# Performance work log

Measured on AMD Instinct MI355X. Metric: run time of the kernel, lower is better.

Reference implementation:

```python
import jax, jax.numpy as jnp
import numpy as np

NEG_INF = 1e9  # matches module's -1000000000.0 masking constant


def setup_inputs() -> dict:
    key = jax.random.key(0)
    kq, kv = jax.random.split(key)
    B, T, D = 4, 2048, 1024
    query = jax.random.normal(kq, (B, T, D), dtype=jnp.float32)
    value = jax.random.normal(kv, (B, T, D), dtype=jnp.float32)
    return {"query": query, "value": value}


def reference(query, value):
    # key defaults to value (len(inputs) == 2 path)
    k = value
    # dot-product scores (canonical Keras Attention _calculate_scores)
    scores = jnp.einsum("bqd,bkd->bqk", query, k)  # [B, Tq, Tv]
    Tq, Tv = scores.shape[-2], scores.shape[-1]
    # causal lower-triangular mask over last two dims (row >= col)
    causal_mask = jnp.tril(jnp.ones((Tq, Tv), dtype=bool))  # [Tq, Tv]
    # scores -= 1e9 * (~mask), then softmax (eval mode: no dropout)
    scores = scores - NEG_INF * (~causal_mask).astype(scores.dtype)
    weights = jax.nn.softmax(scores, axis=-1)
    result = jnp.einsum("bqv,bvd->bqd", weights, value)
    return result
```

## Files before the change

### kernel.cpp

```cpp
#include <hip/hip_runtime.h>
#include <hip/hip_fp16.h>

typedef _Float16 half8 __attribute__((ext_vector_type(8)));
typedef _Float16 half2v __attribute__((ext_vector_type(2)));
typedef float    floatx4 __attribute__((ext_vector_type(4)));

#define MFMA16(a, b, c) __builtin_amdgcn_mfma_f32_16x16x32_f16((a), (b), (c), 0, 0, 0)

constexpr int T_ = 2048;
constexpr int D_ = 1024;
constexpr int NB = 4;
constexpr int NTILE = 136;
constexpr size_t TILE_ELEMS = 16384;

__device__ __forceinline__ half8 cvt8(floatx4 a, floatx4 b) {
  half8 h;
  h[0] = (_Float16)a[0]; h[1] = (_Float16)a[1]; h[2] = (_Float16)a[2]; h[3] = (_Float16)a[3];
  h[4] = (_Float16)b[0]; h[5] = (_Float16)b[1]; h[6] = (_Float16)b[2]; h[7] = (_Float16)b[3];
  return h;
}

__device__ __forceinline__ void gl16(const void* g, void* l) {
  __builtin_amdgcn_global_load_lds(
      (const __attribute__((address_space(1))) void*)g,
      (__attribute__((address_space(3))) void*)l, 16, 0, 0);
}

__global__ __launch_bounds__(256) void cast_q(const float* __restrict__ Q,
                                              _Float16* __restrict__ Qh) {
  const size_t e = ((size_t)blockIdx.x * 256 + threadIdx.x) * 8;
  const int t = (int)(e >> 10);
  const int c = (int)((e >> 3) & 127);
  const int cd = (c & ~7) | ((c ^ t) & 7);
  half8 h = cvt8(*(const floatx4*)(Q + e), *(const floatx4*)(Q + e + 4));
  *(half8*)(Qh + ((size_t)t << 10) + (cd << 3)) = h;
}

__global__ __launch_bounds__(256) void build_vt(const float* __restrict__ V,
                                                _Float16* __restrict__ VhT) {
  __shared__ _Float16 tile[64][65];
  const int bid = blockIdx.x;
  const int b = bid & 3, tt = (bid >> 2) & 31, dd = bid >> 7;
  const float* Vb = V + ((size_t)b * T_ + tt * 64) * D_ + dd * 64;
#pragma unroll
  for (int k = 0; k < 16; ++k) {
    const int e = k * 256 + threadIdx.x, r = e >> 6, c = e & 63;
    tile[r][c] = (_Float16)Vb[(size_t)r * D_ + c];
  }
  __syncthreads();
#pragma unroll
  for (int k = 0; k < 16; ++k) {
    const int e = k * 256 + threadIdx.x, dr = e >> 6, tc = e & 63;
    const int tcd = ((((tc >> 3) ^ dr) & 7) << 3) | (tc & 7);
    VhT[((size_t)b * D_ + dd * 64 + dr) * T_ + tt * 64 + tcd] = tile[tc][dr];
  }
}

__global__ __launch_bounds__(256, 3) void sgemm(const _Float16* __restrict__ Qh,
                                                const float* __restrict__ V,
                                                float* __restrict__ Sp) {
  __shared__ __align__(16) char As[16384];
  __shared__ __align__(16) char Bs[32768];
  const int tid = threadIdx.x;
  const int w = tid >> 6, l = tid & 63, l15 = l & 15, hi = l >> 4;
  const int wr = (w >> 1) * 64, wc = (w & 1) * 64;

  const int b = (int)(blockIdx.x & 3);
  int rem = (int)(blockIdx.x >> 2), j = 0;
  while (rem >= 16 - j) { rem -= 16 - j; ++j; }
  const int i = j + rem;

  const int arow = w * 32 + (l >> 3);
  const int brow = w * 32 + (l >> 4);
  const _Float16* Asrc = Qh + ((size_t)(b * T_ + i * 128 + arow)) * D_ + (l & 7) * 8;
  const float* Bb = V + ((size_t)(b * T_ + j * 128 + brow)) * D_;
  const int lc0 = (l & 8) | ((l & 7) ^ (l >> 4));
  char* Adst = As + w * 4096;
  char* Bdst = Bs + w * 8192;

  floatx4 acc[4][4];
#pragma unroll
  for (int mi = 0; mi < 4; ++mi)
#pragma unroll
    for (int ni = 0; ni < 4; ++ni) acc[mi][ni] = (floatx4){0.f, 0.f, 0.f, 0.f};

  for (int s = 0; s < 16; ++s) {
#pragma unroll
    for (int q = 0; q < 4; ++q)
      gl16(Asrc + (size_t)q * 8 * D_ + s * 64, Adst + q * 1024);
#pragma unroll
    for (int q = 0; q < 8; ++q)
      gl16(Bb + (size_t)q * 4 * D_ + s * 64 + (lc0 ^ ((q & 1) << 2)) * 4,
           Bdst + q * 1024);
    __syncthreads();
#pragma unroll
    for (int s32 = 0; s32 < 2; ++s32) {
      half8 af[4], bb[4];
#pragma unroll
      for (int mi = 0; mi < 4; ++mi) {
        const int row = wr + mi * 16 + l15;
        af[mi] = *(const half8*)(As + row * 128 + ((((s32 << 2) | hi) ^ (row & 7)) << 4));
      }
#pragma unroll
      for (int ni = 0; ni < 4; ++ni) {
        const int row = wc + ni * 16 + l15;
        const int p0 = (s32 << 3) | (((hi << 1) ^ row) & 7);
        const floatx4 f0 = *(const floatx4*)(Bs + row * 256 + (p0 << 4));
        const floatx4 f1 = *(const floatx4*)(Bs + row * 256 + ((p0 ^ 1) << 4));
        bb[ni] = cvt8(f0, f1);
      }
#pragma unroll
      for (int mi = 0; mi < 4; ++mi)
#pragma unroll
        for (int ni = 0; ni < 4; ++ni)
          acc[mi][ni] = MFMA16(af[mi], bb[ni], acc[mi][ni]);
    }
    __syncthreads();
  }

  float* tp = Sp + (size_t)(b * NTILE + ((i * (i + 1)) >> 1) + j) * TILE_ELEMS;
#pragma unroll
  for (int mi = 0; mi < 4; ++mi)
#pragma unroll
    for (int r = 0; r < 4; ++r) {
      const int row = wr + mi * 16 + 4 * hi + r;
#pragma unroll
      for (int ni = 0; ni < 4; ++ni)
        tp[row * 128 + wc + ni * 16 + l15] = acc[mi][ni][r];
    }
}

__global__ __launch_bounds__(256) void smax(float* __restrict__ Sp,
                                            float* __restrict__ lrow) {
  const int b = (int)(blockIdx.x & 3), t = (int)(blockIdx.x >> 2);
  const int i = 15 - (t >> 5), rg = t & 31;
  const int w = threadIdx.x >> 6, l = threadIdx.x & 63;
  const int r = rg * 4 + w, m = i * 128 + r, len = m + 1;
  char* tb0 = (char*)(Sp + (size_t)(b * NTILE + ((i * (i + 1)) >> 1)) * TILE_ELEMS);

  float mx = -1e30f;
  for (int j = 0; j <= i; ++j) {
    const float* tp = (const float*)(tb0 + (size_t)j * 65536) + r * 128 + l * 2;
    const float v0 = tp[0], v1 = tp[1];
    const int col = j * 128 + l * 2;
    if (col < len) mx = fmaxf(mx, v0);
    if (col + 1 < len) mx = fmaxf(mx, v1);
  }
#pragma unroll
  for (int off = 1; off < 64; off <<= 1) mx = fmaxf(mx, __shfl_xor(mx, off));

  const int ch = (l >> 2) & 7, hf = l >> 5;
  const unsigned pb = (unsigned)(r * 512 + hf * 128 + ((ch ^ (r & 7)) << 4) + (l & 3) * 4);
  float sum = 0.f;
  for (int j = 0; j <= i; ++j) {
    char* tbj = tb0 + (size_t)j * 65536;
    const float* tp = (const float*)tbj + r * 128 + l * 2;
    const float v0 = tp[0], v1 = tp[1];
    const int col = j * 128 + l * 2;
    const float p0 = (col < len) ? __expf(v0 - mx) : 0.f;
    const float p1 = (col + 1 < len) ? __expf(v1 - mx) : 0.f;
    sum += p0 + p1;
    half2v hv; hv[0] = (_Float16)p0; hv[1] = (_Float16)p1;
    *(half2v*)(tbj + pb) = hv;
  }
#pragma unroll
  for (int off = 1; off < 64; off <<= 1) sum += __shfl_xor(sum, off);
  if (l == 0) lrow[b * 2048 + m] = sum;
}

__global__ __launch_bounds__(256, 3) void pv(const float* __restrict__ Sp,
                                             const _Float16* __restrict__ VhT,
                                             const float* __restrict__ lrow,
                                             float* __restrict__ O) {
  __shared__ __align__(16) char As[16384];
  __shared__ __align__(16) char Bs[16384];
  __shared__ float Lsh[128];
  const int tid = threadIdx.x;
  const int w = tid >> 6, l = tid & 63, l15 = l & 15, hi = l >> 4;
  const int wr = (w >> 1) * 64, wc = (w & 1) * 64;

  const int b = (int)(blockIdx.x & 3), t = (int)(blockIdx.x >> 2);
  const int r_ = t >> 3;
  const int i = (r_ < 8) ? (15 - r_) : (r_ - 8);
  const int nc = t & 7;
  const int ns = (i + 1) * 2;

  const char* Pbase = (const char*)(Sp + (size_t)(b * NTILE + ((i * (i + 1)) >> 1)) * TILE_ELEMS);
  const int arow = w * 32 + (l >> 3);
  const _Float16* Bsrc = VhT + ((size_t)(b * D_ + nc * 128 + arow)) * T_ + (l & 7) * 8;
  char* Adst = As + w * 4096;
  char* Bdst = Bs + w * 4096;
  if (tid < 128) Lsh[tid] = lrow[b * 2048 + i * 128 + tid];

  floatx4 acc[4][4];
#pragma unroll
  for (int mi = 0; mi < 4; ++mi)
#pragma unroll
    for (int ni = 0; ni < 4; ++ni) acc[mi][ni] = (floatx4){0.f, 0.f, 0.f, 0.f};

  for (int s = 0; s < ns; ++s) {
#pragma unroll
    for (int q = 0; q < 4; ++q)
      gl16(Pbase + (size_t)(s >> 1) * 65536 + (size_t)(arow + q * 8) * 512 +
               (s & 1) * 128 + (l & 7) * 16,
           Adst + q * 1024);
#pragma unroll
    for (int q = 0; q < 4; ++q)
      gl16(Bsrc + (size_t)q * 8 * T_ + s * 64, Bdst + q * 1024);
    __syncthreads();
#pragma unroll
    for (int s32 = 0; s32 < 2; ++s32) {
      half8 af[4], bb[4];
#pragma unroll
      for (int mi = 0; mi < 4; ++mi) {
        const int row = wr + mi * 16 + l15;
        af[mi] = *(const half8*)(As + row * 128 + ((((s32 << 2) | hi) ^ (row & 7)) << 4));
      }
#pragma unroll
      for (int ni = 0; ni < 4; ++ni) {
        const int row = wc + ni * 16 + l15;
        bb[ni] = *(const half8*)(Bs + row * 128 + ((((s32 << 2) | hi) ^ (row & 7)) << 4));
      }
#pragma unroll
      for (int mi = 0; mi < 4; ++mi)
#pragma unroll
        for (int ni = 0; ni < 4; ++ni)
          acc[mi][ni] = MFMA16(af[mi], bb[ni], acc[mi][ni]);
    }
    __syncthreads();
  }

  float* Ob = O + ((size_t)b * T_ + i * 128) * D_ + nc * 128;
#pragma unroll
  for (int mi = 0; mi < 4; ++mi)
#pragma unroll
    for (int r = 0; r < 4; ++r) {
      const int rl = wr + mi * 16 + 4 * hi + r;
      const float inv = 1.0f / Lsh[rl];
#pragma unroll
      for (int ni = 0; ni < 4; ++ni)
        Ob[(size_t)rl * D_ + wc + ni * 16 + l15] = acc[mi][ni][r] * inv;
    }
}

__global__ __launch_bounds__(256) void attn_fb(const float* __restrict__ Q,
                                               const float* __restrict__ V,
                                               float* __restrict__ O) {
  __shared__ float sc[2048];
  __shared__ float red[4];
  const int b = (int)(blockIdx.x >> 11), m = (int)(blockIdx.x & 2047);
  const int tid = threadIdx.x;
  const float* Qr = Q + ((size_t)b * T_ + m) * D_;
  for (int kv = tid; kv <= m; kv += 256) {
    const float* Vr = V + ((size_t)b * T_ + kv) * D_;
    float s = 0.f;
    for (int d = 0; d < D_; d += 4) {
      floatx4 q4 = *(const floatx4*)(Qr + d), v4 = *(const floatx4*)(Vr + d);
      s += q4[0] * v4[0] + q4[1] * v4[1] + q4[2] * v4[2] + q4[3] * v4[3];
    }
    sc[kv] = s;
  }
  __syncthreads();
  float mx = -1e30f;
  for (int kv = tid; kv <= m; kv += 256) mx = fmaxf(mx, sc[kv]);
#pragma unroll
  for (int off = 1; off < 64; off <<= 1) mx = fmaxf(mx, __shfl_xor(mx, off));
  if ((tid & 63) == 0) red[tid >> 6] = mx;
  __syncthreads();
  mx = fmaxf(fmaxf(red[0], red[1]), fmaxf(red[2], red[3]));
  __syncthreads();
  float sum = 0.f;
  for (int kv = tid; kv <= m; kv += 256) { float p = __expf(sc[kv] - mx); sc[kv] = p; sum += p; }
#pragma unroll
  for (int off = 1; off < 64; off <<= 1) sum += __shfl_xor(sum, off);
  __syncthreads();
  if ((tid & 63) == 0) red[tid >> 6] = sum;
  __syncthreads();
  const float inv = 1.0f / (red[0] + red[1] + red[2] + red[3]);
  float* Or = O + ((size_t)b * T_ + m) * D_;
  const int d = tid * 4;
  floatx4 o = {0.f, 0.f, 0.f, 0.f};
  for (int kv = 0; kv <= m; ++kv) {
    const float p = sc[kv];
    const floatx4 v4 = *(const floatx4*)(V + ((size_t)b * T_ + kv) * D_ + d);
    o[0] += p * v4[0]; o[1] += p * v4[1]; o[2] += p * v4[2]; o[3] += p * v4[3];
  }
  o[0] *= inv; o[1] *= inv; o[2] *= inv; o[3] *= inv;
  *(floatx4*)(Or + d) = o;
}

extern "C" void kernel_launch(void* const* d_in, const int* in_sizes, int n_in,
                              void* d_out, int out_size, void* d_ws, size_t ws_size,
                              hipStream_t stream) {
  const float* q = (const float*)d_in[0];
  const float* v = (const float*)d_in[1];
  float* out = (float*)d_out;

  const size_t OFF_S = 16777216;
  const size_t OFF_L = OFF_S + (size_t)NB * NTILE * TILE_ELEMS * 4;
  const size_t NEED = OFF_L + (size_t)NB * 2048 * 4;

  if (ws_size >= NEED) {
    _Float16* fh = (_Float16*)d_ws;
    float* Sp = (float*)((char*)d_ws + OFF_S);
    float* lr = (float*)((char*)d_ws + OFF_L);
    cast_q<<<dim3(4096), dim3(256), 0, stream>>>(q, fh);
    sgemm<<<dim3(NB * NTILE), dim3(256), 0, stream>>>(fh, v, Sp);
    smax<<<dim3(2048), dim3(256), 0, stream>>>(Sp, lr);
    build_vt<<<dim3(2048), dim3(256), 0, stream>>>(v, fh);
    pv<<<dim3(512), dim3(256), 0, stream>>>(Sp, fh, lr, out);
  } else {
    attn_fb<<<dim3(NB * T_), dim3(256), 0, stream>>>(q, v, out);
  }
}
```

Before: 110.4 us.

## Double-buffer LDS in sgemm and pv with 32-wide K steps; widen smax rows

Both GEMM kernels now use a two-stage LDS ping-pong with smaller 32-element K slices, so the global-to-LDS loads for the next step are issued before computing the current one, with a single waitcnt-plus-barrier per step. The swizzle moves from the cast/transpose kernels into the LDS load addressing. The softmax kernel processes two rows per wave with float4 loads and half4 stores, using half as many blocks. The aim is to hide global load latency and cut barrier count per unit of work, at the cost of more loop iterations and new swizzle indexing that must match between the writers and the readers.

```diff
diff --git a/kernel.cpp b/kernel.cpp
--- a/kernel.cpp
+++ b/kernel.cpp
@@ -2,7 +2,7 @@
 #include <hip/hip_fp16.h>
 
 typedef _Float16 half8 __attribute__((ext_vector_type(8)));
-typedef _Float16 half2v __attribute__((ext_vector_type(2)));
+typedef _Float16 half4v __attribute__((ext_vector_type(4)));
 typedef float    floatx4 __attribute__((ext_vector_type(4)));
 
 #define MFMA16(a, b, c) __builtin_amdgcn_mfma_f32_16x16x32_f16((a), (b), (c), 0, 0, 0)
@@ -26,14 +26,16 @@
       (__attribute__((address_space(3))) void*)l, 16, 0, 0);
 }
 
+__device__ __forceinline__ void STEP_SYNC() {
+  asm volatile("s_waitcnt vmcnt(0)" ::: "memory");
+  __builtin_amdgcn_s_barrier();
+  __builtin_amdgcn_sched_barrier(0);
+}
+
 __global__ __launch_bounds__(256) void cast_q(const float* __restrict__ Q,
                                               _Float16* __restrict__ Qh) {
-  const size_t e = ((size_t)blockIdx.x * 256 + threadIdx.x) * 8;
-  const int t = (int)(e >> 10);
-  const int c = (int)((e >> 3) & 127);
-  const int cd = (c & ~7) | ((c ^ t) & 7);
-  half8 h = cvt8(*(const floatx4*)(Q + e), *(const floatx4*)(Q + e + 4));
-  *(half8*)(Qh + ((size_t)t << 10) + (cd << 3)) = h;
+  const size_t i = ((size_t)blockIdx.x * 256 + threadIdx.x) * 8;
+  *(half8*)(Qh + i) = cvt8(*(const floatx4*)(Q + i), *(const floatx4*)(Q + i + 4));
 }
 
 __global__ __launch_bounds__(256) void build_vt(const float* __restrict__ V,
@@ -51,32 +53,42 @@
 #pragma unroll
   for (int k = 0; k < 16; ++k) {
     const int e = k * 256 + threadIdx.x, dr = e >> 6, tc = e & 63;
-    const int tcd = ((((tc >> 3) ^ dr) & 7) << 3) | (tc & 7);
-    VhT[((size_t)b * D_ + dd * 64 + dr) * T_ + tt * 64 + tcd] = tile[tc][dr];
+    VhT[((size_t)b * D_ + dd * 64 + dr) * T_ + tt * 64 + tc] = tile[tc][dr];
   }
 }
 
 __global__ __launch_bounds__(256, 3) void sgemm(const _Float16* __restrict__ Qh,
                                                 const float* __restrict__ V,
                                                 float* __restrict__ Sp) {
-  __shared__ __align__(16) char As[16384];
-  __shared__ __align__(16) char Bs[32768];
+  __shared__ __align__(16) char lds[49152];
   const int tid = threadIdx.x;
   const int w = tid >> 6, l = tid & 63, l15 = l & 15, hi = l >> 4;
   const int wr = (w >> 1) * 64, wc = (w & 1) * 64;
+  const int l2 = l >> 2, l3 = l >> 3;
 
   const int b = (int)(blockIdx.x & 3);
   int rem = (int)(blockIdx.x >> 2), j = 0;
   while (rem >= 16 - j) { rem -= 16 - j; ++j; }
   const int i = j + rem;
 
-  const int arow = w * 32 + (l >> 3);
-  const int brow = w * 32 + (l >> 4);
-  const _Float16* Asrc = Qh + ((size_t)(b * T_ + i * 128 + arow)) * D_ + (l & 7) * 8;
-  const float* Bb = V + ((size_t)(b * T_ + j * 128 + brow)) * D_;
-  const int lc0 = (l & 8) | ((l & 7) ^ (l >> 4));
-  char* Adst = As + w * 4096;
-  char* Bdst = Bs + w * 8192;
+  const _Float16* Qb = Qh + ((size_t)(b * T_ + i * 128)) * D_;
+  const float*    Vb = V  + ((size_t)(b * T_ + j * 128)) * D_;
+
+  auto STAGE = [&](const int s, const int buf) {
+    char* Ad = lds + buf * 24576 + w * 2048;
+    char* Bd = lds + buf * 24576 + 8192 + w * 4096;
+#pragma unroll
+    for (int q = 0; q < 2; ++q) {
+      const int ar = w * 32 + q * 16 + l2;
+      const int sw = (ar + (ar >> 2)) & 3;
+      gl16(Qb + (size_t)ar * D_ + s * 32 + (((l & 3) ^ sw) << 3), Ad + q * 1024);
+    }
+#pragma unroll
+    for (int q = 0; q < 4; ++q) {
+      const int br = w * 32 + q * 8 + l3;
+      gl16(Vb + (size_t)br * D_ + s * 32 + (((l & 7) ^ (br & 7)) << 2), Bd + q * 1024);
+    }
+  };
 
   floatx4 acc[4][4];
 #pragma unroll
@@ -84,38 +96,34 @@
 #pragma unroll
     for (int ni = 0; ni < 4; ++ni) acc[mi][ni] = (floatx4){0.f, 0.f, 0.f, 0.f};
 
-  for (int s = 0; s < 16; ++s) {
-#pragma unroll
-    for (int q = 0; q < 4; ++q)
-      gl16(Asrc + (size_t)q * 8 * D_ + s * 64, Adst + q * 1024);
-#pragma unroll
-    for (int q = 0; q < 8; ++q)
-      gl16(Bb + (size_t)q * 4 * D_ + s * 64 + (lc0 ^ ((q & 1) << 2)) * 4,
-           Bdst + q * 1024);
-    __syncthreads();
-#pragma unroll
-    for (int s32 = 0; s32 < 2; ++s32) {
-      half8 af[4], bb[4];
-#pragma unroll
-      for (int mi = 0; mi < 4; ++mi) {
-        const int row = wr + mi * 16 + l15;
-        af[mi] = *(const half8*)(As + row * 128 + ((((s32 << 2) | hi) ^ (row & 7)) << 4));
-      }
-#pragma unroll
-      for (int ni = 0; ni < 4; ++ni) {
-        const int row = wc + ni * 16 + l15;
-        const int p0 = (s32 << 3) | (((hi << 1) ^ row) & 7);
-        const floatx4 f0 = *(const floatx4*)(Bs + row * 256 + (p0 << 4));
-        const floatx4 f1 = *(const floatx4*)(Bs + row * 256 + ((p0 ^ 1) << 4));
-        bb[ni] = cvt8(f0, f1);
-      }
-#pragma unroll
-      for (int mi = 0; mi < 4; ++mi)
-#pragma unroll
-        for (int ni = 0; ni < 4; ++ni)
-          acc[mi][ni] = MFMA16(af[mi], bb[ni], acc[mi][ni]);
-    }
-    __syncthreads();
+  STAGE(0, 0);
+  STEP_SYNC();
+  for (int s = 0; s < 32; ++s) {
+    const int buf = s & 1;
+    if (s + 1 < 32) STAGE(s + 1, buf ^ 1);
+    const char* Ab = lds + buf * 24576;
+    const char* Bb = lds + buf * 24576 + 8192;
+    half8 af[4], bb[4];
+#pragma unroll
+    for (int mi = 0; mi < 4; ++mi) {
+      const int row = wr + mi * 16 + l15;
+      const int sw = (row + (row >> 2)) & 3;
+      af[mi] = *(const half8*)(Ab + row * 64 + ((hi ^ sw) << 4));
+    }
+#pragma unroll
+    for (int ni = 0; ni < 4; ++ni) {
+      const int row = wc + ni * 16 + l15;
+      const int p0 = (hi << 1) ^ (row & 7);
+      const floatx4 f0 = *(const floatx4*)(Bb + row * 128 + (p0 << 4));
+      const floatx4 f1 = *(const floatx4*)(Bb + row * 128 + ((p0 ^ 1) << 4));
+      bb[ni] = cvt8(f0, f1);
+    }
+#pragma unroll
+    for (int mi = 0; mi < 4; ++mi)
+#pragma unroll
+      for (int ni = 0; ni < 4; ++ni)
+        acc[mi][ni] = MFMA16(af[mi], bb[ni], acc[mi][ni]);
+    STEP_SYNC();
   }
 
   float* tp = Sp + (size_t)(b * NTILE + ((i * (i + 1)) >> 1) + j) * TILE_ELEMS;
@@ -133,101 +141,109 @@
 __global__ __launch_bounds__(256) void smax(float* __restrict__ Sp,
                                             float* __restrict__ lrow) {
   const int b = (int)(blockIdx.x & 3), t = (int)(blockIdx.x >> 2);
-  const int i = 15 - (t >> 5), rg = t & 31;
-  const int w = threadIdx.x >> 6, l = threadIdx.x & 63;
-  const int r = rg * 4 + w, m = i * 128 + r, len = m + 1;
+  const int wv = threadIdx.x >> 6, l = threadIdx.x & 63;
+  const int l32 = l & 31;
+  const int row = 2040 - t * 8 + wv * 2 + (l >> 5);
+  const int i = row >> 7, r = row & 127;
   char* tb0 = (char*)(Sp + (size_t)(b * NTILE + ((i * (i + 1)) >> 1)) * TILE_ELEMS);
 
   float mx = -1e30f;
   for (int j = 0; j <= i; ++j) {
-    const float* tp = (const float*)(tb0 + (size_t)j * 65536) + r * 128 + l * 2;
-    const float v0 = tp[0], v1 = tp[1];
-    const int col = j * 128 + l * 2;
-    if (col < len) mx = fmaxf(mx, v0);
-    if (col + 1 < len) mx = fmaxf(mx, v1);
-  }
-#pragma unroll
-  for (int off = 1; off < 64; off <<= 1) mx = fmaxf(mx, __shfl_xor(mx, off));
-
-  const int ch = (l >> 2) & 7, hf = l >> 5;
-  const unsigned pb = (unsigned)(r * 512 + hf * 128 + ((ch ^ (r & 7)) << 4) + (l & 3) * 4);
+    const floatx4 v = *(const floatx4*)(tb0 + (size_t)j * 65536 + r * 512 + l32 * 16);
+    const int col0 = j * 128 + l32 * 4;
+#pragma unroll
+    for (int e = 0; e < 4; ++e)
+      if (col0 + e <= row) mx = fmaxf(mx, v[e]);
+  }
+#pragma unroll
+  for (int off = 1; off < 32; off <<= 1) mx = fmaxf(mx, __shfl_xor(mx, off));
+
   float sum = 0.f;
   for (int j = 0; j <= i; ++j) {
     char* tbj = tb0 + (size_t)j * 65536;
-    const float* tp = (const float*)tbj + r * 128 + l * 2;
-    const float v0 = tp[0], v1 = tp[1];
-    const int col = j * 128 + l * 2;
-    const float p0 = (col < len) ? __expf(v0 - mx) : 0.f;
-    const float p1 = (col + 1 < len) ? __expf(v1 - mx) : 0.f;
-    sum += p0 + p1;
-    half2v hv; hv[0] = (_Float16)p0; hv[1] = (_Float16)p1;
-    *(half2v*)(tbj + pb) = hv;
-  }
-#pragma unroll
-  for (int off = 1; off < 64; off <<= 1) sum += __shfl_xor(sum, off);
-  if (l == 0) lrow[b * 2048 + m] = sum;
+    const floatx4 v = *(const floatx4*)(tbj + r * 512 + l32 * 16);
+    const int col0 = j * 128 + l32 * 4;
+    half4v hv;
+#pragma unroll
+    for (int e = 0; e < 4; ++e) {
+      const float p = (col0 + e <= row) ? __expf(v[e] - mx) : 0.f;
+      sum += p;
+      hv[e] = (_Float16)p;
+    }
+    *(half4v*)(tbj + r * 512 + l32 * 8) = hv;
+  }
+#pragma unroll
+  for (int off = 1; off < 32; off <<= 1) sum += __shfl_xor(sum, off);
+  if (l32 == 0) lrow[b * 2048 + row] = sum;
 }
 
 __global__ __launch_bounds__(256, 3) void pv(const float* __restrict__ Sp,
                                              const _Float16* __restrict__ VhT,
                                              const float* __restrict__ lrow,
                                              float* __restrict__ O) {
-  __shared__ __align__(16) char As[16384];
-  __shared__ __align__(16) char Bs[16384];
+  __shared__ __align__(16) char lds[32768];
   __shared__ float Lsh[128];
   const int tid = threadIdx.x;
   const int w = tid >> 6, l = tid & 63, l15 = l & 15, hi = l >> 4;
   const int wr = (w >> 1) * 64, wc = (w & 1) * 64;
+  const int l2 = l >> 2;
 
   const int b = (int)(blockIdx.x & 3), t = (int)(blockIdx.x >> 2);
   const int r_ = t >> 3;
   const int i = (r_ < 8) ? (15 - r_) : (r_ - 8);
   const int nc = t & 7;
-  const int ns = (i + 1) * 2;
+  const int ns = (i + 1) * 4;
 
   const char* Pbase = (const char*)(Sp + (size_t)(b * NTILE + ((i * (i + 1)) >> 1)) * TILE_ELEMS);
-  const int arow = w * 32 + (l >> 3);
-  const _Float16* Bsrc = VhT + ((size_t)(b * D_ + nc * 128 + arow)) * T_ + (l & 7) * 8;
-  char* Adst = As + w * 4096;
-  char* Bdst = Bs + w * 4096;
+  const _Float16* Vt = VhT + ((size_t)(b * D_ + nc * 128)) * T_;
   if (tid < 128) Lsh[tid] = lrow[b * 2048 + i * 128 + tid];
 
+  auto STAGE = [&](const int s, const int buf) {
+    char* Ad = lds + buf * 16384 + w * 2048;
+    char* Bd = lds + buf * 16384 + 8192 + w * 2048;
+#pragma unroll
+    for (int q = 0; q < 2; ++q) {
+      const int ar = w * 32 + q * 16 + l2;
+      const int sw = (ar + (ar >> 2)) & 3;
+      gl16(Pbase + (size_t)(s >> 2) * 65536 + ar * 512 + (s & 3) * 64 +
+               (((l & 3) ^ sw) << 4),
+           Ad + q * 1024);
+      gl16(Vt + (size_t)ar * T_ + s * 32 + (((l & 3) ^ sw) << 3), Bd + q * 1024);
+    }
+  };
+
   floatx4 acc[4][4];
 #pragma unroll
   for (int mi = 0; mi < 4; ++mi)
 #pragma unroll
     for (int ni = 0; ni < 4; ++ni) acc[mi][ni] = (floatx4){0.f, 0.f, 0.f, 0.f};
 
+  STAGE(0, 0);
+  STEP_SYNC();
   for (int s = 0; s < ns; ++s) {
-#pragma unroll
-    for (int q = 0; q < 4; ++q)
-      gl16(Pbase + (size_t)(s >> 1) * 65536 + (size_t)(arow + q * 8) * 512 +
-               (s & 1) * 128 + (l & 7) * 16,
-           Adst + q * 1024);
-#pragma unroll
-    for (int q = 0; q < 4; ++q)
-      gl16(Bsrc + (size_t)q * 8 * T_ + s * 64, Bdst + q * 1024);
-    __syncthreads();
-#pragma unroll
-    for (int s32 = 0; s32 < 2; ++s32) {
-      half8 af[4], bb[4];
-#pragma unroll
-      for (int mi = 0; mi < 4; ++mi) {
-        const int row = wr + mi * 16 + l15;
-        af[mi] = *(const half8*)(As + row * 128 + ((((s32 << 2) | hi) ^ (row & 7)) << 4));
-      }
-#pragma unroll
-      for (int ni = 0; ni < 4; ++ni) {
-        const int row = wc + ni * 16 + l15;
-        bb[ni] = *(const half8*)(Bs + row * 128 + ((((s32 << 2) | hi) ^ (row & 7)) << 4));
-      }
-#pragma unroll
-      for (int mi = 0; mi < 4; ++mi)
-#pragma unroll
-        for (int ni = 0; ni < 4; ++ni)
-          acc[mi][ni] = MFMA16(af[mi], bb[ni], acc[mi][ni]);
-    }
-    __syncthreads();
+    const int buf = s & 1;
+    if (s + 1 < ns) STAGE(s + 1, buf ^ 1);
+    const char* Ab = lds + buf * 16384;
+    const char* Bb = lds + buf * 16384 + 8192;
+    half8 af[4], bb[4];
+#pragma unroll
+    for (int mi = 0; mi < 4; ++mi) {
+      const int row = wr + mi * 16 + l15;
+      const int sw = (row + (row >> 2)) & 3;
+      af[mi] = *(const half8*)(Ab + row * 64 + ((hi ^ sw) << 4));
+    }
+#pragma unroll
+    for (int ni = 0; ni < 4; ++ni) {
+      const int row = wc + ni * 16 + l15;
+      const int sw = (row + (row >> 2)) & 3;
+      bb[ni] = *(const half8*)(Bb + row * 64 + ((hi ^ sw) << 4));
+    }
+#pragma unroll
+    for (int mi = 0; mi < 4; ++mi)
+#pragma unroll
+      for (int ni = 0; ni < 4; ++ni)
+        acc[mi][ni] = MFMA16(af[mi], bb[ni], acc[mi][ni]);
+    STEP_SYNC();
   }
 
   float* Ob = O + ((size_t)b * T_ + i * 128) * D_ + nc * 128;
@@ -306,7 +322,7 @@
     float* lr = (float*)((char*)d_ws + OFF_L);
     cast_q<<<dim3(4096), dim3(256), 0, stream>>>(q, fh);
     sgemm<<<dim3(NB * NTILE), dim3(256), 0, stream>>>(fh, v, Sp);
-    smax<<<dim3(2048), dim3(256), 0, stream>>>(Sp, lr);
+    smax<<<dim3(1024), dim3(256), 0, stream>>>(Sp, lr);
     build_vt<<<dim3(2048), dim3(256), 0, stream>>>(v, fh);
     pv<<<dim3(512), dim3(256), 0, stream>>>(Sp, fh, lr, out);
   } else {
```

Result: slower. 113.8 us (+3.1%).

## Fuse per-tile softmax into score GEMM and rescale tiles with a combine pass

Applied to the files above, without the earlier changes.

The score GEMM now computes a per-tile row max and row sum, applies the causal mask on diagonal tiles, and writes fp16 exponentiated probabilities straight from its registers. This removes the fp32 score round-trip and the separate softmax kernel. A small combine kernel merges the per-tile statistics into per-tile rescale factors and inverse row sums, which the PV kernel applies to its A operand on load. V is also pre-cast to fp16, and both GEMMs switch to 128-wide K steps with a 16-way swizzle, 64KB of dynamic LDS and occupancy 2. The trade-offs are an extra cast pass and an extra kernel launch, plus some precision loss from scaling fp16 probabilities by fp16 factors.

```diff
diff --git a/kernel.cpp b/kernel.cpp
--- a/kernel.cpp
+++ b/kernel.cpp
@@ -2,8 +2,8 @@
 #include <hip/hip_fp16.h>
 
 typedef _Float16 half8 __attribute__((ext_vector_type(8)));
-typedef _Float16 half2v __attribute__((ext_vector_type(2)));
 typedef float    floatx4 __attribute__((ext_vector_type(4)));
+typedef unsigned int uintx4 __attribute__((ext_vector_type(4)));
 
 #define MFMA16(a, b, c) __builtin_amdgcn_mfma_f32_16x16x32_f16((a), (b), (c), 0, 0, 0)
 
@@ -11,7 +11,7 @@
 constexpr int D_ = 1024;
 constexpr int NB = 4;
 constexpr int NTILE = 136;
-constexpr size_t TILE_ELEMS = 16384;
+constexpr size_t PT_ELEMS = 16384;
 
 __device__ __forceinline__ half8 cvt8(floatx4 a, floatx4 b) {
   half8 h;
@@ -26,14 +26,10 @@
       (__attribute__((address_space(3))) void*)l, 16, 0, 0);
 }
 
-__global__ __launch_bounds__(256) void cast_q(const float* __restrict__ Q,
-                                              _Float16* __restrict__ Qh) {
-  const size_t e = ((size_t)blockIdx.x * 256 + threadIdx.x) * 8;
-  const int t = (int)(e >> 10);
-  const int c = (int)((e >> 3) & 127);
-  const int cd = (c & ~7) | ((c ^ t) & 7);
-  half8 h = cvt8(*(const floatx4*)(Q + e), *(const floatx4*)(Q + e + 4));
-  *(half8*)(Qh + ((size_t)t << 10) + (cd << 3)) = h;
+__global__ __launch_bounds__(256) void cast_h(const float* __restrict__ X,
+                                              _Float16* __restrict__ Xh) {
+  const size_t i = ((size_t)blockIdx.x * 256 + threadIdx.x) * 8;
+  *(half8*)(Xh + i) = cvt8(*(const floatx4*)(X + i), *(const floatx4*)(X + i + 4));
 }
 
 __global__ __launch_bounds__(256) void build_vt(const float* __restrict__ V,
@@ -51,16 +47,18 @@
 #pragma unroll
   for (int k = 0; k < 16; ++k) {
     const int e = k * 256 + threadIdx.x, dr = e >> 6, tc = e & 63;
-    const int tcd = ((((tc >> 3) ^ dr) & 7) << 3) | (tc & 7);
-    VhT[((size_t)b * D_ + dd * 64 + dr) * T_ + tt * 64 + tcd] = tile[tc][dr];
-  }
-}
-
-__global__ __launch_bounds__(256, 3) void sgemm(const _Float16* __restrict__ Qh,
-                                                const float* __restrict__ V,
-                                                float* __restrict__ Sp) {
-  __shared__ __align__(16) char As[16384];
-  __shared__ __align__(16) char Bs[32768];
+    VhT[((size_t)b * D_ + dd * 64 + dr) * T_ + tt * 64 + tc] = tile[tc][dr];
+  }
+}
+
+__global__ __launch_bounds__(256, 2) void sgemm(const _Float16* __restrict__ Qh,
+                                                const _Float16* __restrict__ Vh,
+                                                _Float16* __restrict__ Pt,
+                                                float* __restrict__ mg,
+                                                float* __restrict__ lg) {
+  extern __shared__ __align__(16) char lds[];
+  char* As = lds;
+  char* Bs = lds + 32768;
   const int tid = threadIdx.x;
   const int w = tid >> 6, l = tid & 63, l15 = l & 15, hi = l >> 4;
   const int wr = (w >> 1) * 64, wc = (w & 1) * 64;
@@ -70,12 +68,10 @@
   while (rem >= 16 - j) { rem -= 16 - j; ++j; }
   const int i = j + rem;
 
-  const int arow = w * 32 + (l >> 3);
-  const int brow = w * 32 + (l >> 4);
-  const _Float16* Asrc = Qh + ((size_t)(b * T_ + i * 128 + arow)) * D_ + (l & 7) * 8;
-  const float* Bb = V + ((size_t)(b * T_ + j * 128 + brow)) * D_;
-  const int lc0 = (l & 8) | ((l & 7) ^ (l >> 4));
-  char* Adst = As + w * 4096;
+  const _Float16* Qb = Qh + ((size_t)(b * T_ + i * 128)) * D_;
+  const _Float16* Vb = Vh + ((size_t)(b * T_ + j * 128)) * D_;
+  const int srow = w * 32 + (l >> 4);
+  char* Adst = As + w * 8192;
   char* Bdst = Bs + w * 8192;
 
   floatx4 acc[4][4];
@@ -84,30 +80,27 @@
 #pragma unroll
     for (int ni = 0; ni < 4; ++ni) acc[mi][ni] = (floatx4){0.f, 0.f, 0.f, 0.f};
 
-  for (int s = 0; s < 16; ++s) {
-#pragma unroll
-    for (int q = 0; q < 4; ++q)
-      gl16(Asrc + (size_t)q * 8 * D_ + s * 64, Adst + q * 1024);
-#pragma unroll
-    for (int q = 0; q < 8; ++q)
-      gl16(Bb + (size_t)q * 4 * D_ + s * 64 + (lc0 ^ ((q & 1) << 2)) * 4,
-           Bdst + q * 1024);
+  for (int s = 0; s < 8; ++s) {
+#pragma unroll
+    for (int q = 0; q < 8; ++q) {
+      const int r0 = srow + q * 4;
+      const int sc = ((l & 15) ^ (r0 & 15)) * 8;
+      gl16(Qb + (size_t)r0 * D_ + s * 128 + sc, Adst + q * 1024);
+      gl16(Vb + (size_t)r0 * D_ + s * 128 + sc, Bdst + q * 1024);
+    }
     __syncthreads();
 #pragma unroll
-    for (int s32 = 0; s32 < 2; ++s32) {
+    for (int s32 = 0; s32 < 4; ++s32) {
       half8 af[4], bb[4];
 #pragma unroll
       for (int mi = 0; mi < 4; ++mi) {
         const int row = wr + mi * 16 + l15;
-        af[mi] = *(const half8*)(As + row * 128 + ((((s32 << 2) | hi) ^ (row & 7)) << 4));
+        af[mi] = *(const half8*)(As + row * 256 + (((s32 * 4 + hi) ^ (row & 15)) << 4));
       }
 #pragma unroll
       for (int ni = 0; ni < 4; ++ni) {
         const int row = wc + ni * 16 + l15;
-        const int p0 = (s32 << 3) | (((hi << 1) ^ row) & 7);
-        const floatx4 f0 = *(const floatx4*)(Bs + row * 256 + (p0 << 4));
-        const floatx4 f1 = *(const floatx4*)(Bs + row * 256 + ((p0 ^ 1) << 4));
-        bb[ni] = cvt8(f0, f1);
+        bb[ni] = *(const half8*)(Bs + row * 256 + (((s32 * 4 + hi) ^ (row & 15)) << 4));
       }
 #pragma unroll
       for (int mi = 0; mi < 4; ++mi)
@@ -118,63 +111,126 @@
     __syncthreads();
   }
 
-  float* tp = Sp + (size_t)(b * NTILE + ((i * (i + 1)) >> 1) + j) * TILE_ELEMS;
-#pragma unroll
-  for (int mi = 0; mi < 4; ++mi)
-#pragma unroll
-    for (int r = 0; r < 4; ++r) {
-      const int row = wr + mi * 16 + 4 * hi + r;
-#pragma unroll
-      for (int ni = 0; ni < 4; ++ni)
-        tp[row * 128 + wc + ni * 16 + l15] = acc[mi][ni][r];
-    }
-}
-
-__global__ __launch_bounds__(256) void smax(float* __restrict__ Sp,
-                                            float* __restrict__ lrow) {
-  const int b = (int)(blockIdx.x & 3), t = (int)(blockIdx.x >> 2);
-  const int i = 15 - (t >> 5), rg = t & 31;
-  const int w = threadIdx.x >> 6, l = threadIdx.x & 63;
-  const int r = rg * 4 + w, m = i * 128 + r, len = m + 1;
-  char* tb0 = (char*)(Sp + (size_t)(b * NTILE + ((i * (i + 1)) >> 1)) * TILE_ELEMS);
-
-  float mx = -1e30f;
+  float* Mex = (float*)Bs;
+  float* Lex = (float*)(Bs + 1024);
+
+  if (i == j) {
+#pragma unroll
+    for (int mi = 0; mi < 4; ++mi)
+#pragma unroll
+      for (int ni = 0; ni < 4; ++ni) {
+        const int col = wc + ni * 16 + l15;
+        const int row0 = wr + mi * 16 + 4 * hi;
+#pragma unroll
+        for (int r = 0; r < 4; ++r)
+          if (col > row0 + r) acc[mi][ni][r] = -1e30f;
+      }
+  }
+
+  floatx4 mrow[4];
+#pragma unroll
+  for (int mi = 0; mi < 4; ++mi) {
+#pragma unroll
+    for (int r = 0; r < 4; ++r)
+      mrow[mi][r] = fmaxf(fmaxf(acc[mi][0][r], acc[mi][1][r]),
+                          fmaxf(acc[mi][2][r], acc[mi][3][r]));
+#pragma unroll
+    for (int off = 1; off < 16; off <<= 1)
+#pragma unroll
+      for (int r = 0; r < 4; ++r)
+        mrow[mi][r] = fmaxf(mrow[mi][r], __shfl_xor(mrow[mi][r], off));
+  }
+  if (l15 == 0) {
+#pragma unroll
+    for (int mi = 0; mi < 4; ++mi)
+      *(floatx4*)&Mex[(w & 1) * 128 + wr + mi * 16 + 4 * hi] = mrow[mi];
+  }
+  __syncthreads();
+#pragma unroll
+  for (int mi = 0; mi < 4; ++mi) {
+    const floatx4 m0 = *(const floatx4*)&Mex[wr + mi * 16 + 4 * hi];
+    const floatx4 m1 = *(const floatx4*)&Mex[128 + wr + mi * 16 + 4 * hi];
+#pragma unroll
+    for (int r = 0; r < 4; ++r) mrow[mi][r] = fmaxf(m0[r], m1[r]);
+  }
+
+  floatx4 lsum[4];
+#pragma unroll
+  for (int mi = 0; mi < 4; ++mi) {
+    lsum[mi] = (floatx4){0.f, 0.f, 0.f, 0.f};
+    const int row0 = wr + mi * 16 + 4 * hi;
+#pragma unroll
+    for (int ni = 0; ni < 4; ++ni) {
+      const int col = wc + ni * 16 + l15;
+#pragma unroll
+      for (int r = 0; r < 4; ++r) {
+        const float p = __expf(acc[mi][ni][r] - mrow[mi][r]);
+        lsum[mi][r] += p;
+        *(_Float16*)(As + (row0 + r) * 256 + col * 2) = (_Float16)p;
+      }
+    }
+#pragma unroll
+    for (int off = 1; off < 16; off <<= 1)
+#pragma unroll
+      for (int r = 0; r < 4; ++r) lsum[mi][r] += __shfl_xor(lsum[mi][r], off);
+  }
+  if (l15 == 0) {
+#pragma unroll
+    for (int mi = 0; mi < 4; ++mi)
+      *(floatx4*)&Lex[(w & 1) * 128 + wr + mi * 16 + 4 * hi] = lsum[mi];
+  }
+  __syncthreads();
+
+  if (((w & 1) == 0) && l15 == 0) {
+    const size_t base = ((size_t)(b * 16 + j)) * 2048 + i * 128;
+#pragma unroll
+    for (int mi = 0; mi < 4; ++mi) {
+      const int r0 = wr + mi * 16 + 4 * hi;
+      const floatx4 l0 = *(const floatx4*)&Lex[r0];
+      const floatx4 l1 = *(const floatx4*)&Lex[128 + r0];
+#pragma unroll
+      for (int r = 0; r < 4; ++r) {
+        mg[base + r0 + r] = mrow[mi][r];
+        lg[base + r0 + r] = l0[r] + l1[r];
+      }
+    }
+  }
+  _Float16* Pg = Pt + (size_t)(b * NTILE + ((i * (i + 1)) >> 1) + j) * PT_ELEMS;
+  const int drow = tid >> 1, dhalf = tid & 1;
+#pragma unroll
+  for (int k = 0; k < 8; ++k) {
+    const int c = k ^ (tid & 7);
+    const uintx4 v = *(const uintx4*)(As + drow * 256 + dhalf * 128 + c * 16);
+    *(uintx4*)((char*)Pg + drow * 256 + dhalf * 128 + c * 16) = v;
+  }
+}
+
+__global__ __launch_bounds__(256) void combine(const float* __restrict__ mg,
+                                               const float* __restrict__ lg,
+                                               _Float16* __restrict__ ah,
+                                               float* __restrict__ linv) {
+  const int gid = (int)(blockIdx.x * 256 + threadIdx.x);
+  const int b = gid >> 11, row = gid & 2047, i = row >> 7;
+  const size_t mb = (size_t)b * 32768 + row;
+  float M = -1e30f;
+  for (int j = 0; j <= i; ++j) M = fmaxf(M, mg[mb + (size_t)j * 2048]);
+  float L = 0.f;
   for (int j = 0; j <= i; ++j) {
-    const float* tp = (const float*)(tb0 + (size_t)j * 65536) + r * 128 + l * 2;
-    const float v0 = tp[0], v1 = tp[1];
-    const int col = j * 128 + l * 2;
-    if (col < len) mx = fmaxf(mx, v0);
-    if (col + 1 < len) mx = fmaxf(mx, v1);
-  }
-#pragma unroll
-  for (int off = 1; off < 64; off <<= 1) mx = fmaxf(mx, __shfl_xor(mx, off));
-
-  const int ch = (l >> 2) & 7, hf = l >> 5;
-  const unsigned pb = (unsigned)(r * 512 + hf * 128 + ((ch ^ (r & 7)) << 4) + (l & 3) * 4);
-  float sum = 0.f;
-  for (int j = 0; j <= i; ++j) {
-    char* tbj = tb0 + (size_t)j * 65536;
-    const float* tp = (const float*)tbj + r * 128 + l * 2;
-    const float v0 = tp[0], v1 = tp[1];
-    const int col = j * 128 + l * 2;
-    const float p0 = (col < len) ? __expf(v0 - mx) : 0.f;
-    const float p1 = (col + 1 < len) ? __expf(v1 - mx) : 0.f;
-    sum += p0 + p1;
-    half2v hv; hv[0] = (_Float16)p0; hv[1] = (_Float16)p1;
-    *(half2v*)(tbj + pb) = hv;
-  }
-#pragma unroll
-  for (int off = 1; off < 64; off <<= 1) sum += __shfl_xor(sum, off);
-  if (l == 0) lrow[b * 2048 + m] = sum;
-}
-
-__global__ __launch_bounds__(256, 3) void pv(const float* __restrict__ Sp,
+    const float a = __expf(mg[mb + (size_t)j * 2048] - M);
+    L += a * lg[mb + (size_t)j * 2048];
+    ah[((size_t)b * 2048 + row) * 16 + j] = (_Float16)a;
+  }
+  linv[b * 2048 + row] = 1.0f / L;
+}
+
+__global__ __launch_bounds__(256, 2) void pv(const _Float16* __restrict__ Pt,
                                              const _Float16* __restrict__ VhT,
-                                             const float* __restrict__ lrow,
+                                             const _Float16* __restrict__ ah,
+                                             const float* __restrict__ linv,
                                              float* __restrict__ O) {
-  __shared__ __align__(16) char As[16384];
-  __shared__ __align__(16) char Bs[16384];
-  __shared__ float Lsh[128];
+  extern __shared__ __align__(16) char lds[];
+  char* As = lds;
+  char* Bs = lds + 32768;
   const int tid = threadIdx.x;
   const int w = tid >> 6, l = tid & 63, l15 = l & 15, hi = l >> 4;
   const int wr = (w >> 1) * 64, wc = (w & 1) * 64;
@@ -183,14 +239,13 @@
   const int r_ = t >> 3;
   const int i = (r_ < 8) ? (15 - r_) : (r_ - 8);
   const int nc = t & 7;
-  const int ns = (i + 1) * 2;
-
-  const char* Pbase = (const char*)(Sp + (size_t)(b * NTILE + ((i * (i + 1)) >> 1)) * TILE_ELEMS);
-  const int arow = w * 32 + (l >> 3);
-  const _Float16* Bsrc = VhT + ((size_t)(b * D_ + nc * 128 + arow)) * T_ + (l & 7) * 8;
-  char* Adst = As + w * 4096;
-  char* Bdst = Bs + w * 4096;
-  if (tid < 128) Lsh[tid] = lrow[b * 2048 + i * 128 + tid];
+  const int ns = i + 1;
+
+  const _Float16* Pb = Pt + (size_t)(b * NTILE + ((i * (i + 1)) >> 1)) * PT_ELEMS;
+  const _Float16* Vt = VhT + ((size_t)(b * D_ + nc * 128)) * T_;
+  const int srow = w * 32 + (l >> 4);
+  char* Adst = As + w * 8192;
+  char* Bdst = Bs + w * 8192;
 
   floatx4 acc[4][4];
 #pragma unroll
@@ -199,27 +254,31 @@
     for (int ni = 0; ni < 4; ++ni) acc[mi][ni] = (floatx4){0.f, 0.f, 0.f, 0.f};
 
   for (int s = 0; s < ns; ++s) {
-#pragma unroll
-    for (int q = 0; q < 4; ++q)
-      gl16(Pbase + (size_t)(s >> 1) * 65536 + (size_t)(arow + q * 8) * 512 +
-               (s & 1) * 128 + (l & 7) * 16,
-           Adst + q * 1024);
-#pragma unroll
-    for (int q = 0; q < 4; ++q)
-      gl16(Bsrc + (size_t)q * 8 * T_ + s * 64, Bdst + q * 1024);
+    _Float16 aw[4];
+#pragma unroll
+    for (int mi = 0; mi < 4; ++mi)
+      aw[mi] = ah[((size_t)(b * 2048 + i * 128 + wr + mi * 16 + l15)) * 16 + s];
+#pragma unroll
+    for (int q = 0; q < 8; ++q) {
+      const int r0 = srow + q * 4;
+      const int sc = ((l & 15) ^ (r0 & 15)) * 8;
+      gl16(Pb + (size_t)s * PT_ELEMS + (size_t)r0 * 128 + sc, Adst + q * 1024);
+      gl16(Vt + (size_t)r0 * T_ + s * 128 + sc, Bdst + q * 1024);
+    }
     __syncthreads();
 #pragma unroll
-    for (int s32 = 0; s32 < 2; ++s32) {
+    for (int s32 = 0; s32 < 4; ++s32) {
       half8 af[4], bb[4];
 #pragma unroll
       for (int mi = 0; mi < 4; ++mi) {
         const int row = wr + mi * 16 + l15;
-        af[mi] = *(const half8*)(As + row * 128 + ((((s32 << 2) | hi) ^ (row & 7)) << 4));
+        af[mi] = *(const half8*)(As + row * 256 + (((s32 * 4 + hi) ^ (row & 15)) << 4));
+        af[mi] *= aw[mi];
       }
 #pragma unroll
       for (int ni = 0; ni < 4; ++ni) {
         const int row = wc + ni * 16 + l15;
-        bb[ni] = *(const half8*)(Bs + row * 128 + ((((s32 << 2) | hi) ^ (row & 7)) << 4));
+        bb[ni] = *(const half8*)(Bs + row * 256 + (((s32 * 4 + hi) ^ (row & 15)) << 4));
       }
 #pragma unroll
       for (int mi = 0; mi < 4; ++mi)
@@ -236,10 +295,10 @@
 #pragma unroll
     for (int r = 0; r < 4; ++r) {
       const int rl = wr + mi * 16 + 4 * hi + r;
-      const float inv = 1.0f / Lsh[rl];
+      const float iv = linv[b * 2048 + i * 128 + rl];
 #pragma unroll
       for (int ni = 0; ni < 4; ++ni)
-        Ob[(size_t)rl * D_ + wc + ni * 16 + l15] = acc[mi][ni][r] * inv;
+        Ob[(size_t)rl * D_ + wc + ni * 16 + l15] = acc[mi][ni][r] * iv;
     }
 }
 
@@ -296,19 +355,30 @@
   const float* v = (const float*)d_in[1];
   float* out = (float*)d_out;
 
-  const size_t OFF_S = 16777216;
-  const size_t OFF_L = OFF_S + (size_t)NB * NTILE * TILE_ELEMS * 4;
-  const size_t NEED = OFF_L + (size_t)NB * 2048 * 4;
+  const size_t OFF_VH = 16777216;
+  const size_t OFF_P  = 33554432;
+  const size_t OFF_M  = OFF_P + (size_t)NB * NTILE * PT_ELEMS * 2;
+  const size_t OFF_LT = OFF_M + 524288;
+  const size_t OFF_AH = OFF_LT + 524288;
+  const size_t OFF_LI = OFF_AH + 262144;
+  const size_t NEED   = OFF_LI + 32768;
 
   if (ws_size >= NEED) {
-    _Float16* fh = (_Float16*)d_ws;
-    float* Sp = (float*)((char*)d_ws + OFF_S);
-    float* lr = (float*)((char*)d_ws + OFF_L);
-    cast_q<<<dim3(4096), dim3(256), 0, stream>>>(q, fh);
-    sgemm<<<dim3(NB * NTILE), dim3(256), 0, stream>>>(fh, v, Sp);
-    smax<<<dim3(2048), dim3(256), 0, stream>>>(Sp, lr);
-    build_vt<<<dim3(2048), dim3(256), 0, stream>>>(v, fh);
-    pv<<<dim3(512), dim3(256), 0, stream>>>(Sp, fh, lr, out);
+    _Float16* qh = (_Float16*)d_ws;
+    _Float16* vh = (_Float16*)((char*)d_ws + OFF_VH);
+    _Float16* pt = (_Float16*)((char*)d_ws + OFF_P);
+    float* mg = (float*)((char*)d_ws + OFF_M);
+    float* lg = (float*)((char*)d_ws + OFF_LT);
+    _Float16* ah = (_Float16*)((char*)d_ws + OFF_AH);
+    float* li = (float*)((char*)d_ws + OFF_LI);
+    hipFuncSetAttribute((const void*)sgemm, hipFuncAttributeMaxDynamicSharedMemorySize, 65536);
+    hipFuncSetAttribute((const void*)pv, hipFuncAttributeMaxDynamicSharedMemorySize, 65536);
+    cast_h<<<dim3(4096), dim3(256), 0, stream>>>(q, qh);
+    cast_h<<<dim3(4096), dim3(256), 0, stream>>>(v, vh);
+    sgemm<<<dim3(NB * NTILE), dim3(256), 65536, stream>>>(qh, vh, pt, mg, lg);
+    combine<<<dim3(32), dim3(256), 0, stream>>>(mg, lg, ah, li);
+    build_vt<<<dim3(2048), dim3(256), 0, stream>>>(v, qh);
+    pv<<<dim3(512), dim3(256), 65536, stream>>>(pt, qh, ah, li, out);
   } else {
     attn_fb<<<dim3(NB * T_), dim3(256), 0, stream>>>(q, v, out);
   }
```

After: 118.2 us. 7.0% more time.
